# Kernel optimization log

Measured on AMD Instinct MI355X. Metric: run time of the kernel, lower is better.

The kernel has to match this reference:

```python
import jax, jax.numpy as jnp
import numpy as np

EMB = 1024
HEAD = 64  # emb_size // head_nb = 1024 // 16

def setup_inputs() -> dict:
    key = jax.random.key(0)
    kx, kq, kk, kv = jax.random.split(key, 4)
    x = jax.random.normal(kx, (8, 2048, EMB), dtype=jnp.float32)
    # torch nn.Linear(EMB, HEAD) weight has shape [HEAD, EMB]; y = x @ W.T
    s = 1.0 / np.sqrt(EMB)
    Wq = jax.random.uniform(kq, (HEAD, EMB), jnp.float32, -s, s)
    Wk = jax.random.uniform(kk, (HEAD, EMB), jnp.float32, -s, s)
    Wv = jax.random.uniform(kv, (HEAD, EMB), jnp.float32, -s, s)
    return {"x": x, "Wq": Wq, "Wk": Wk, "Wv": Wv}

def reference(x, Wq, Wk, Wv):
    B, T, C = x.shape
    q = jnp.einsum('btc,hc->bth', x, Wq)  # [B,T,H]
    k = jnp.einsum('btc,hc->bth', x, Wk)
    v = jnp.einsum('btc,hc->bth', x, Wv)
    scale = 1.0 / jnp.sqrt(jnp.float32(q.shape[-1]))
    wei = jnp.einsum('bth,bsh->bts', q, k) * scale  # [B,T,T]
    causal = jnp.tril(jnp.ones((T, T), dtype=bool))
    wei = jnp.where(causal, wei, -jnp.inf)
    wei = jax.nn.softmax(wei, axis=-1)
    # dropout is identity in eval mode
    out = jnp.einsum('bts,bsh->bth', wei, v)  # [B,T,H]
    return out
```

## Files before the change

### kernel.cpp

```cpp
#include <hip/hip_runtime.h>
#include <math.h>

#define SEQ  2048
#define NROW 16384
#define HEAD 64
#define EMB  1024

typedef __attribute__((ext_vector_type(8))) short short8;
typedef __attribute__((ext_vector_type(4))) float f32x4;

static __device__ __forceinline__ unsigned short f2bf(float f) {
    unsigned u = __builtin_bit_cast(unsigned, f);
    u += 0x7fffu + ((u >> 16) & 1u);
    return (unsigned short)(u >> 16);
}
static __device__ __forceinline__ float bf2f(unsigned short u) {
    unsigned v = (unsigned)u << 16;
    return __builtin_bit_cast(float, v);
}
static __device__ __forceinline__ short8 cvt8(float4 a, float4 b) {
    short8 r;
    r[0] = f2bf(a.x); r[1] = f2bf(a.y); r[2] = f2bf(a.z); r[3] = f2bf(a.w);
    r[4] = f2bf(b.x); r[5] = f2bf(b.y); r[6] = f2bf(b.z); r[7] = f2bf(b.w);
    return r;
}

__global__ __launch_bounds__(256) void wcvt_kernel(
    const float* __restrict__ Wq, const float* __restrict__ Wk,
    const float* __restrict__ Wv, unsigned short* __restrict__ Wb)
{
    const int idx = (blockIdx.x * 256 + threadIdx.x) * 4;
    const int h = idx >> 10;
    const float* src;
    if (h < 64)       src = Wq + idx;
    else if (h < 128) src = Wk + (idx - 65536);
    else              src = Wv + (idx - 131072);
    float4 f = *(const float4*)src;
    ushort4 o;
    o.x = f2bf(f.x); o.y = f2bf(f.y); o.z = f2bf(f.z); o.w = f2bf(f.w);
    *(ushort4*)(Wb + idx) = o;
}

__global__ __launch_bounds__(256, 4) void qkv_mfma_kernel(
    const float* __restrict__ x, const unsigned short* __restrict__ Wb,
    unsigned short* __restrict__ qN, unsigned short* __restrict__ kN,
    unsigned short* __restrict__ vT)
{
    __shared__ float          As[32][66];
    __shared__ unsigned short Bs[96][68];

    const int tid   = threadIdx.x;
    const int w     = tid >> 6;
    const int lane  = tid & 63;
    const int col   = lane & 15;
    const int quad  = lane >> 4;
    const int mhalf = w >> 1;
    const int ntri  = w & 1;
    const int row0  = blockIdx.x * 32;
    const int ny    = blockIdx.y;

    f32x4 acc[3];
#pragma unroll
    for (int t = 0; t < 3; ++t) acc[t] = (f32x4){0.f, 0.f, 0.f, 0.f};

    for (int k0 = 0; k0 < EMB; k0 += 64) {
        __syncthreads();
#pragma unroll
        for (int rd = 0; rd < 2; ++rd) {
            int flat = rd * 256 + tid;
            int r = flat >> 4, c = flat & 15;
            float4 v = *(const float4*)(x + (size_t)(row0 + r) * EMB + k0 + c * 4);
            *(float4*)&As[r][c * 4] = v;
        }
#pragma unroll
        for (int rd = 0; rd < 3; ++rd) {
            int flat = rd * 256 + tid;
            int h = flat >> 3, c = flat & 7;
            short8 v = *(const short8*)(Wb + (size_t)(ny * 96 + h) * EMB + k0 + c * 8);
            *(short8*)&Bs[h][c * 8] = v;
        }
        __syncthreads();
#pragma unroll
        for (int ks = 0; ks < 2; ++ks) {
            float4 a0 = *(const float4*)&As[mhalf * 16 + col][ks * 32 + quad * 8];
            float4 a1 = *(const float4*)&As[mhalf * 16 + col][ks * 32 + quad * 8 + 4];
            short8 af = cvt8(a0, a1);
#pragma unroll
            for (int t = 0; t < 3; ++t) {
                short8 bf = *(const short8*)&Bs[ntri * 48 + 16 * t + col][ks * 32 + quad * 8];
                acc[t] = __builtin_amdgcn_mfma_f32_16x16x32_bf16(af, bf, acc[t], 0, 0, 0);
            }
        }
    }

#pragma unroll
    for (int t = 0; t < 3; ++t) {
        const int hb = ny * 96 + ntri * 48 + 16 * t;
        const int h  = hb + col;
        const int ro = row0 + mhalf * 16 + quad * 4;
        if (hb < 64) {
#pragma unroll
            for (int r = 0; r < 4; ++r)
                qN[(size_t)(ro + r) * HEAD + h] = f2bf(acc[t][r]);
        } else if (hb < 128) {
#pragma unroll
            for (int r = 0; r < 4; ++r)
                kN[(size_t)(ro + r) * HEAD + (h - 64)] = f2bf(acc[t][r]);
        } else {
            ushort4 uv;
            uv.x = f2bf(acc[t][0]); uv.y = f2bf(acc[t][1]);
            uv.z = f2bf(acc[t][2]); uv.w = f2bf(acc[t][3]);
            *(ushort4*)(vT + (size_t)(h - 128) * NROW + ro) = uv;
        }
    }
}

__global__ __launch_bounds__(256, 2) void attn_kernel(
    const unsigned short* __restrict__ qN,
    const unsigned short* __restrict__ kN,
    const unsigned short* __restrict__ vT,
    unsigned short* __restrict__ op,
    float2* __restrict__ ml)
{
    __shared__ unsigned short Ks[64][68];
    __shared__ unsigned short Vs[64][68];
    __shared__ float Pl[4][16][68];

    const int qt   = 31 - (int)blockIdx.x;
    const int b    = blockIdx.y;
    const int p    = blockIdx.z;
    const int tid  = threadIdx.x;
    const int wv   = tid >> 6;
    const int lane = tid & 63;
    const int col  = lane & 15;
    const int quad = lane >> 4;

    const int q0   = qt * 64 + wv * 16;
    const int q0g  = b * SEQ + q0;
    const int Cb   = qt + 1;
    const int half = (Cb + 1) >> 1;
    const int kt0  = p ? half : 0;
    const int kt1  = p ? Cb : half;

    const short8* qp8 = (const short8*)qN + (size_t)(q0g + col) * 8;
    short8 aq0 = qp8[quad];
    short8 aq1 = qp8[quad + 4];

    f32x4 o[4];
#pragma unroll
    for (int t = 0; t < 4; ++t) o[t] = (f32x4){0.f, 0.f, 0.f, 0.f};
    float m_i[4], l_i[4];
#pragma unroll
    for (int r = 0; r < 4; ++r) { m_i[r] = -INFINITY; l_i[r] = 0.0f; }

    for (int kt = kt0; kt < kt1; ++kt) {
        const int s0  = kt * 64;
        const int s0g = b * SEQ + s0;
        const bool diag = (kt == Cb - 1);

        __syncthreads();
#pragma unroll
        for (int rd = 0; rd < 2; ++rd) {
            int flat = rd * 256 + tid;
            int r = flat >> 3, c = flat & 7;
            *(short8*)&Ks[r][c * 8] =
                *(const short8*)(kN + (size_t)(s0g + r) * HEAD + c * 8);
        }
#pragma unroll
        for (int rd = 0; rd < 2; ++rd) {
            int flat = rd * 256 + tid;
            int h = flat >> 3, c = flat & 7;
            *(short8*)&Vs[h][c * 8] =
                *(const short8*)(vT + (size_t)h * NROW + s0g + c * 8);
        }
        __syncthreads();

        f32x4 sv[4];
#pragma unroll
        for (int t = 0; t < 4; ++t) {
            short8 kf0 = *(const short8*)&Ks[16 * t + col][quad * 8];
            short8 kf1 = *(const short8*)&Ks[16 * t + col][32 + quad * 8];
            sv[t] = (f32x4){0.f, 0.f, 0.f, 0.f};
            sv[t] = __builtin_amdgcn_mfma_f32_16x16x32_bf16(aq0, kf0, sv[t], 0, 0, 0);
            sv[t] = __builtin_amdgcn_mfma_f32_16x16x32_bf16(aq1, kf1, sv[t], 0, 0, 0);
        }

        float pv[4][4];
#pragma unroll
        for (int r = 0; r < 4; ++r) {
            const int grow = q0 + quad * 4 + r;
            float rm = -INFINITY;
#pragma unroll
            for (int t = 0; t < 4; ++t) {
                float val = sv[t][r] * 0.125f;
                if (diag && (s0 + 16 * t + col > grow)) val = -INFINITY;
                pv[t][r] = val;
                rm = fmaxf(rm, val);
            }
            rm = fmaxf(rm, __shfl_xor(rm, 1, 16));
            rm = fmaxf(rm, __shfl_xor(rm, 2, 16));
            rm = fmaxf(rm, __shfl_xor(rm, 4, 16));
            rm = fmaxf(rm, __shfl_xor(rm, 8, 16));
            const float mnew  = fmaxf(m_i[r], rm);
            const float alpha = __expf(m_i[r] - mnew);
            m_i[r] = mnew;
            float ls = 0.0f;
#pragma unroll
            for (int t = 0; t < 4; ++t) {
                float e = __expf(pv[t][r] - mnew);
                pv[t][r] = e;
                ls += e;
            }
            ls += __shfl_xor(ls, 1, 16);
            ls += __shfl_xor(ls, 2, 16);
            ls += __shfl_xor(ls, 4, 16);
            ls += __shfl_xor(ls, 8, 16);
            l_i[r] = l_i[r] * alpha + ls;
#pragma unroll
            for (int tn = 0; tn < 4; ++tn) o[tn][r] *= alpha;
        }

#pragma unroll
        for (int t = 0; t < 4; ++t)
#pragma unroll
            for (int r = 0; r < 4; ++r)
                Pl[wv][quad * 4 + r][16 * t + col] = pv[t][r];
        short8 pf[2];
#pragma unroll
        for (int st = 0; st < 2; ++st) {
            float4 pa = *(const float4*)&Pl[wv][col][quad * 8 + 32 * st];
            float4 pb = *(const float4*)&Pl[wv][col][quad * 8 + 32 * st + 4];
            pf[st] = cvt8(pa, pb);
        }

#pragma unroll
        for (int tn = 0; tn < 4; ++tn) {
            short8 vf0 = *(const short8*)&Vs[16 * tn + col][quad * 8];
            short8 vf1 = *(const short8*)&Vs[16 * tn + col][32 + quad * 8];
            o[tn] = __builtin_amdgcn_mfma_f32_16x16x32_bf16(pf[0], vf0, o[tn], 0, 0, 0);
            o[tn] = __builtin_amdgcn_mfma_f32_16x16x32_bf16(pf[1], vf1, o[tn], 0, 0, 0);
        }
    }

#pragma unroll
    for (int tn = 0; tn < 4; ++tn)
#pragma unroll
        for (int r = 0; r < 4; ++r)
            op[(size_t)(p * NROW + q0g + quad * 4 + r) * HEAD + 16 * tn + col] =
                f2bf(o[tn][r]);
    if (col == 0) {
#pragma unroll
        for (int r = 0; r < 4; ++r)
            ml[p * NROW + q0g + quad * 4 + r] = make_float2(m_i[r], l_i[r]);
    }
}

__global__ __launch_bounds__(256) void merge_kernel(
    const unsigned short* __restrict__ op, const float2* __restrict__ ml,
    float* __restrict__ out)
{
    const int idx = blockIdx.x * 256 + threadIdx.x;
    const int row = idx >> 4;
    const int hc  = (idx & 15) * 4;

    float2 e0 = ml[row];
    float2 e1 = ml[NROW + row];
    float m  = fmaxf(e0.x, e1.x);
    float w0 = (e0.x > -INFINITY) ? __expf(e0.x - m) : 0.0f;
    float w1 = (e1.x > -INFINITY) ? __expf(e1.x - m) : 0.0f;
    float inv = 1.0f / (e0.y * w0 + e1.y * w1);

    ushort4 u0 = *(const ushort4*)(op + (size_t)row * HEAD + hc);
    ushort4 u1 = *(const ushort4*)(op + (size_t)(NROW + row) * HEAD + hc);
    float4 r;
    r.x = (bf2f(u0.x) * w0 + bf2f(u1.x) * w1) * inv;
    r.y = (bf2f(u0.y) * w0 + bf2f(u1.y) * w1) * inv;
    r.z = (bf2f(u0.z) * w0 + bf2f(u1.z) * w1) * inv;
    r.w = (bf2f(u0.w) * w0 + bf2f(u1.w) * w1) * inv;
    *(float4*)(out + (size_t)row * HEAD + hc) = r;
}

extern "C" void kernel_launch(void* const* d_in, const int* in_sizes, int n_in,
                              void* d_out, int out_size, void* d_ws, size_t ws_size,
                              hipStream_t stream)
{
    const float* x  = (const float*)d_in[0];
    const float* Wq = (const float*)d_in[1];
    const float* Wk = (const float*)d_in[2];
    const float* Wv = (const float*)d_in[3];

    char* w = (char*)d_ws;
    unsigned short* qN = (unsigned short*)w;
    unsigned short* kN = (unsigned short*)(w + (2u << 20));
    unsigned short* vT = (unsigned short*)(w + (4u << 20));
    unsigned short* Wb = (unsigned short*)(w + (6u << 20));
    unsigned short* op = (unsigned short*)(w + (6u << 20) + 393216);
    float2*         ml = (float2*)(w + (10u << 20) + 393216);
    float* out = (float*)d_out;

    wcvt_kernel<<<192, 256, 0, stream>>>(Wq, Wk, Wv, Wb);
    qkv_mfma_kernel<<<dim3(512, 2), 256, 0, stream>>>(x, Wb, qN, kN, vT);
    attn_kernel<<<dim3(32, 8, 2), 256, 0, stream>>>(qN, kN, vT, op, ml);
    merge_kernel<<<1024, 256, 0, stream>>>(op, ml, out);
}
```

Before: 165.2 us.

## Restructure QKV projection to read x once and load K/V fragments directly

The QKV projection now converts the whole 32-row x tile to bf16 in shared memory once and computes all 192 output columns per block. This halves the grid, so x is read from global memory once instead of twice, and weight fragments are streamed straight from global/L2 with no per-k-step shared staging or barriers. The attention kernel drops its K/V shared-memory tiles and syncthreads, and each wave loads its MFMA fragments directly from global memory. The 1/sqrt(d) scale is folded into Q at projection time. The trade-off is more per-wave global loads, which rely on cache, plus a large shared-memory footprint that limits occupancy in the projection kernel.

```diff
diff --git a/kernel.cpp b/kernel.cpp
--- a/kernel.cpp
+++ b/kernel.cpp
@@ -41,67 +41,59 @@
     *(ushort4*)(Wb + idx) = o;
 }
 
-__global__ __launch_bounds__(256, 4) void qkv_mfma_kernel(
+__global__ __launch_bounds__(256, 2) void qkv_mfma_kernel(
     const float* __restrict__ x, const unsigned short* __restrict__ Wb,
     unsigned short* __restrict__ qN, unsigned short* __restrict__ kN,
     unsigned short* __restrict__ vT)
 {
-    __shared__ float          As[32][66];
-    __shared__ unsigned short Bs[96][68];
-
-    const int tid   = threadIdx.x;
-    const int w     = tid >> 6;
-    const int lane  = tid & 63;
-    const int col   = lane & 15;
-    const int quad  = lane >> 4;
-    const int mhalf = w >> 1;
-    const int ntri  = w & 1;
-    const int row0  = blockIdx.x * 32;
-    const int ny    = blockIdx.y;
-
-    f32x4 acc[3];
-#pragma unroll
-    for (int t = 0; t < 3; ++t) acc[t] = (f32x4){0.f, 0.f, 0.f, 0.f};
-
-    for (int k0 = 0; k0 < EMB; k0 += 64) {
-        __syncthreads();
-#pragma unroll
-        for (int rd = 0; rd < 2; ++rd) {
-            int flat = rd * 256 + tid;
-            int r = flat >> 4, c = flat & 15;
-            float4 v = *(const float4*)(x + (size_t)(row0 + r) * EMB + k0 + c * 4);
-            *(float4*)&As[r][c * 4] = v;
-        }
-#pragma unroll
-        for (int rd = 0; rd < 3; ++rd) {
-            int flat = rd * 256 + tid;
-            int h = flat >> 3, c = flat & 7;
-            short8 v = *(const short8*)(Wb + (size_t)(ny * 96 + h) * EMB + k0 + c * 8);
-            *(short8*)&Bs[h][c * 8] = v;
-        }
-        __syncthreads();
-#pragma unroll
-        for (int ks = 0; ks < 2; ++ks) {
-            float4 a0 = *(const float4*)&As[mhalf * 16 + col][ks * 32 + quad * 8];
-            float4 a1 = *(const float4*)&As[mhalf * 16 + col][ks * 32 + quad * 8 + 4];
-            short8 af = cvt8(a0, a1);
-#pragma unroll
-            for (int t = 0; t < 3; ++t) {
-                short8 bf = *(const short8*)&Bs[ntri * 48 + 16 * t + col][ks * 32 + quad * 8];
-                acc[t] = __builtin_amdgcn_mfma_f32_16x16x32_bf16(af, bf, acc[t], 0, 0, 0);
-            }
-        }
-    }
-
-#pragma unroll
-    for (int t = 0; t < 3; ++t) {
-        const int hb = ny * 96 + ntri * 48 + 16 * t;
+    __shared__ unsigned short xs[32][1032];
+
+    const int tid  = threadIdx.x;
+    const int w    = tid >> 6;
+    const int lane = tid & 63;
+    const int col  = lane & 15;
+    const int quad = lane >> 4;
+    const int mh   = w & 1;
+    const int nh   = w >> 1;
+    const int row0 = blockIdx.x * 32;
+
+#pragma unroll
+    for (int it = 0; it < 16; ++it) {
+        int c  = it * 256 + tid;
+        int rw = c >> 7;
+        int ch = c & 127;
+        const float* p = x + (size_t)(row0 + rw) * EMB + ch * 8;
+        float4 f0 = *(const float4*)p;
+        float4 f1 = *(const float4*)(p + 4);
+        *(short8*)&xs[rw][ch * 8] = cvt8(f0, f1);
+    }
+    __syncthreads();
+
+    const short8* bb = (const short8*)Wb + (size_t)(nh * 96 + col) * 128 + quad;
+
+    f32x4 acc[6];
+#pragma unroll
+    for (int t = 0; t < 6; ++t) acc[t] = (f32x4){0.f, 0.f, 0.f, 0.f};
+
+#pragma unroll 4
+    for (int ks = 0; ks < 32; ++ks) {
+        short8 af = *(const short8*)&xs[mh * 16 + col][ks * 32 + quad * 8];
+#pragma unroll
+        for (int t = 0; t < 6; ++t) {
+            short8 bf = bb[t * 2048 + ks * 4];
+            acc[t] = __builtin_amdgcn_mfma_f32_16x16x32_bf16(af, bf, acc[t], 0, 0, 0);
+        }
+    }
+
+    const int ro = row0 + mh * 16 + quad * 4;
+#pragma unroll
+    for (int t = 0; t < 6; ++t) {
+        const int hb = nh * 96 + 16 * t;
         const int h  = hb + col;
-        const int ro = row0 + mhalf * 16 + quad * 4;
         if (hb < 64) {
 #pragma unroll
             for (int r = 0; r < 4; ++r)
-                qN[(size_t)(ro + r) * HEAD + h] = f2bf(acc[t][r]);
+                qN[(size_t)(ro + r) * HEAD + h] = f2bf(acc[t][r] * 0.125f);
         } else if (hb < 128) {
 #pragma unroll
             for (int r = 0; r < 4; ++r)
@@ -122,8 +114,6 @@
     unsigned short* __restrict__ op,
     float2* __restrict__ ml)
 {
-    __shared__ unsigned short Ks[64][68];
-    __shared__ unsigned short Vs[64][68];
     __shared__ float Pl[4][16][68];
 
     const int qt   = 31 - (int)blockIdx.x;
@@ -158,31 +148,27 @@
         const int s0g = b * SEQ + s0;
         const bool diag = (kt == Cb - 1);
 
-        __syncthreads();
-#pragma unroll
-        for (int rd = 0; rd < 2; ++rd) {
-            int flat = rd * 256 + tid;
-            int r = flat >> 3, c = flat & 7;
-            *(short8*)&Ks[r][c * 8] =
-                *(const short8*)(kN + (size_t)(s0g + r) * HEAD + c * 8);
-        }
-#pragma unroll
-        for (int rd = 0; rd < 2; ++rd) {
-            int flat = rd * 256 + tid;
-            int h = flat >> 3, c = flat & 7;
-            *(short8*)&Vs[h][c * 8] =
-                *(const short8*)(vT + (size_t)h * NROW + s0g + c * 8);
-        }
-        __syncthreads();
+        short8 kf[4][2];
+#pragma unroll
+        for (int t = 0; t < 4; ++t) {
+            const short8* kp8 = (const short8*)kN + (size_t)(s0g + 16 * t + col) * 8;
+            kf[t][0] = kp8[quad];
+            kf[t][1] = kp8[quad + 4];
+        }
+        short8 vf[4][2];
+#pragma unroll
+        for (int tn = 0; tn < 4; ++tn) {
+            const short8* vp8 = (const short8*)vT + (size_t)(16 * tn + col) * 2048 + (s0g >> 3);
+            vf[tn][0] = vp8[quad];
+            vf[tn][1] = vp8[quad + 4];
+        }
 
         f32x4 sv[4];
 #pragma unroll
         for (int t = 0; t < 4; ++t) {
-            short8 kf0 = *(const short8*)&Ks[16 * t + col][quad * 8];
-            short8 kf1 = *(const short8*)&Ks[16 * t + col][32 + quad * 8];
             sv[t] = (f32x4){0.f, 0.f, 0.f, 0.f};
-            sv[t] = __builtin_amdgcn_mfma_f32_16x16x32_bf16(aq0, kf0, sv[t], 0, 0, 0);
-            sv[t] = __builtin_amdgcn_mfma_f32_16x16x32_bf16(aq1, kf1, sv[t], 0, 0, 0);
+            sv[t] = __builtin_amdgcn_mfma_f32_16x16x32_bf16(aq0, kf[t][0], sv[t], 0, 0, 0);
+            sv[t] = __builtin_amdgcn_mfma_f32_16x16x32_bf16(aq1, kf[t][1], sv[t], 0, 0, 0);
         }
 
         float pv[4][4];
@@ -192,7 +178,7 @@
             float rm = -INFINITY;
 #pragma unroll
             for (int t = 0; t < 4; ++t) {
-                float val = sv[t][r] * 0.125f;
+                float val = sv[t][r];
                 if (diag && (s0 + 16 * t + col > grow)) val = -INFINITY;
                 pv[t][r] = val;
                 rm = fmaxf(rm, val);
@@ -235,10 +221,8 @@
 
 #pragma unroll
         for (int tn = 0; tn < 4; ++tn) {
-            short8 vf0 = *(const short8*)&Vs[16 * tn + col][quad * 8];
-            short8 vf1 = *(const short8*)&Vs[16 * tn + col][32 + quad * 8];
-            o[tn] = __builtin_amdgcn_mfma_f32_16x16x32_bf16(pf[0], vf0, o[tn], 0, 0, 0);
-            o[tn] = __builtin_amdgcn_mfma_f32_16x16x32_bf16(pf[1], vf1, o[tn], 0, 0, 0);
+            o[tn] = __builtin_amdgcn_mfma_f32_16x16x32_bf16(pf[0], vf[tn][0], o[tn], 0, 0, 0);
+            o[tn] = __builtin_amdgcn_mfma_f32_16x16x32_bf16(pf[1], vf[tn][1], o[tn], 0, 0, 0);
         }
     }
 
@@ -299,7 +283,7 @@
     float* out = (float*)d_out;
 
     wcvt_kernel<<<192, 256, 0, stream>>>(Wq, Wk, Wv, Wb);
-    qkv_mfma_kernel<<<dim3(512, 2), 256, 0, stream>>>(x, Wb, qN, kN, vT);
+    qkv_mfma_kernel<<<512, 256, 0, stream>>>(x, Wb, qN, kN, vT);
     attn_kernel<<<dim3(32, 8, 2), 256, 0, stream>>>(qN, kN, vT, op, ml);
     merge_kernel<<<1024, 256, 0, stream>>>(op, ml, out);
 }
```

Result: slower. 205.3 us (+24.2%).
